# Kernel optimization log

Measured on AMD Instinct MI355X. Metric: run time of the kernel, lower is better.

The kernel has to match this reference:

```python
import jax, jax.numpy as jnp
import numpy as np

D = 512      # embedding_dimension
L1 = 1024    # english sentence length
L2 = 1024    # french sentence length
V1 = 32000   # english vocab
V2 = 32000   # french vocab
NNEG = 8192  # negative samples
SCALE = 0.05 # param init scale (keeps exp() stable)


def setup_inputs() -> dict:
    key = jax.random.key(0)
    ks = jax.random.split(key, 32)
    def n(k, shape):
        return jax.random.normal(k, shape, dtype=jnp.float32) * SCALE
    inp = {}
    inp["en"] = jax.random.randint(ks[0], (L1,), 0, V1)
    inp["fr"] = jax.random.randint(ks[1], (L2,), 0, V2)
    inp["en_neg"] = jax.random.randint(ks[2], (NNEG,), 0, V1)
    inp["fr_neg"] = jax.random.randint(ks[3], (NNEG,), 0, V2)
    # input embeddings
    inp["emb"] = n(ks[4], (V1, D))
    # 3-layer BiLSTM, hidden=D per direction; layer0 in=D, layers 1-2 in=2D
    inp["Wih0"] = n(ks[5], (2, 4 * D, D)); inp["Whh0"] = n(ks[6], (2, 4 * D, D)); inp["b0"] = n(ks[7], (2, 4 * D))
    inp["Wih1"] = n(ks[8], (2, 4 * D, 2 * D)); inp["Whh1"] = n(ks[9], (2, 4 * D, D)); inp["b1"] = n(ks[10], (2, 4 * D))
    inp["Wih2"] = n(ks[11], (2, 4 * D, 2 * D)); inp["Whh2"] = n(ks[12], (2, 4 * D, D)); inp["b2"] = n(ks[13], (2, 4 * D))
    # inference nets (mu and sigma, 2-layer each)
    inp["Wmu1"] = n(ks[14], (D, D)); inp["bmu1"] = n(ks[15], (D,))
    inp["Wmu2"] = n(ks[16], (D, D)); inp["bmu2"] = n(ks[17], (D,))
    inp["Ws1"] = n(ks[18], (D, D)); inp["bs1"] = n(ks[19], (D,))
    inp["Ws2"] = n(ks[20], (D, D)); inp["bs2"] = n(ks[21], (D,))
    # softmax-approximation embedding tables
    inp["E_en"] = n(ks[22], (V1, D))
    inp["E_fr"] = n(ks[23], (V2, D))
    # reparameterization noise (epsilon.sample() per token, made explicit)
    inp["eps"] = jax.random.normal(ks[24], (L1, D), dtype=jnp.float32)
    return inp


def _lstm_bidir(xs, Wih, Whh, b):
    # xs: (L, in); Wih: (2, 4D, in); Whh: (2, 4D, D); b: (2, 4D)
    def run(d, reverse):
        Wi, Wh, bb = Wih[d], Whh[d], b[d]
        def step(carry, x):
            h, c = carry
            g = Wi @ x + Wh @ h + bb
            i, f, gg, o = jnp.split(g, 4)
            i = jax.nn.sigmoid(i); f = jax.nn.sigmoid(f)
            gg = jnp.tanh(gg); o = jax.nn.sigmoid(o)
            c = f * c + i * gg
            h = o * jnp.tanh(c)
            return (h, c), h
        init = (jnp.zeros((Wh.shape[1],), xs.dtype), jnp.zeros((Wh.shape[1],), xs.dtype))
        _, hs = jax.lax.scan(step, init, xs, reverse=reverse)
        return hs
    return run(0, False), run(1, True)  # each (L, D)


def reference(en, fr, en_neg, fr_neg, emb,
              Wih0, Whh0, b0, Wih1, Whh1, b1, Wih2, Whh2, b2,
              Wmu1, bmu1, Wmu2, bmu2, Ws1, bs1, Ws2, bs2,
              E_en, E_fr, eps):
    x = emb[en]                                   # (L1, D)
    hf, hb = _lstm_bidir(x, Wih0, Whh0, b0)
    hf, hb = _lstm_bidir(jnp.concatenate([hf, hb], -1), Wih1, Whh1, b1)
    hf, hb = _lstm_bidir(jnp.concatenate([hf, hb], -1), Wih2, Whh2, b2)
    h = hf + hb                                   # fwd+bwd hidden sum (intermediate[0][0]+intermediate[0][1])
    mu = jax.nn.relu(h @ Wmu1.T + bmu1) @ Wmu2.T + bmu2
    sigma = jax.nn.softplus(jax.nn.relu(h @ Ws1.T + bs1) @ Ws2.T + bs2)
    z = mu + eps * sigma                          # reparameterized sample (L1, D)
    # closed-form KL( N(mu, diag(sigma^2)) || N(0, I) ), summed over tokens
    kl = 0.5 * jnp.sum(sigma ** 2 + mu ** 2 - 1.0 - 2.0 * jnp.log(sigma))
    # english negative-sampling softmax approximation, summed over tokens
    pos = jnp.exp(jnp.sum(z * E_en[en], axis=-1))            # (L1,)
    neg = jnp.sum(jnp.exp(z @ E_en[en_neg].T), axis=-1)      # (L1,)
    sum_x = jnp.sum(pos / (pos + neg))
    # alignment scoring: every french token vs every english latent z
    s = jnp.exp(z @ E_fr[fr].T)                               # (L1, L2)
    negf = jnp.sum(jnp.exp(z @ E_fr[fr_neg].T), -1, keepdims=True)  # (L1, 1)
    p = s / (s + negf)                                        # (L1, L2)
    sum_y = jnp.sum(p) / L1                                   # uniform-alignment marginal
    return -(sum_x + sum_y - kl)


if __name__ == "__main__":
    out = reference(**setup_inputs())
    print(out)
```

## Files before the change

kernel.cpp:

```cpp
#include <hip/hip_runtime.h>
#include <hip/hip_bf16.h>


template<bool GATHER, bool RELU, int EPI>
__global__ __launch_bounds__(256) void gemm_nt(
    const float* __restrict__ A, const float* __restrict__ B,
    const float* __restrict__ bias, const int* __restrict__ idx,
    float* __restrict__ C, const float* __restrict__ negf,
    float* __restrict__ outsum, int M, int N, int K)
{
    __shared__ float As[16][68];
    __shared__ float Bs[16][68];
    __shared__ float wsum[4];

    const int tid = threadIdx.x;
    const int bm = blockIdx.x, bn = blockIdx.y;
    const int tx = tid & 15, ty = tid >> 4;
    const int lr = tid >> 2;
    const int lk = (tid & 3) * 4;

    const long arow = (long)bm * 64 + lr;
    const int  brow = bn * 64 + lr;
    const long bsrc = GATHER ? (long)idx[brow] : (long)brow;
    const float* Ap = A + arow * K + lk;
    const float* Bp = B + bsrc * K + lk;

    float acc[4][4] = {};

    for (int k0 = 0; k0 < K; k0 += 16) {
        float4 av = *(const float4*)(Ap + k0);
        float4 bv = *(const float4*)(Bp + k0);
        __syncthreads();
        As[lk + 0][lr] = av.x; As[lk + 1][lr] = av.y;
        As[lk + 2][lr] = av.z; As[lk + 3][lr] = av.w;
        Bs[lk + 0][lr] = bv.x; Bs[lk + 1][lr] = bv.y;
        Bs[lk + 2][lr] = bv.z; Bs[lk + 3][lr] = bv.w;
        __syncthreads();
#pragma unroll
        for (int k = 0; k < 16; ++k) {
            float4 a = *(const float4*)&As[k][ty * 4];
            float4 b = *(const float4*)&Bs[k][tx * 4];
            float ar[4] = {a.x, a.y, a.z, a.w};
            float br[4] = {b.x, b.y, b.z, b.w};
#pragma unroll
            for (int i = 0; i < 4; ++i)
#pragma unroll
                for (int j = 0; j < 4; ++j)
                    acc[i][j] += ar[i] * br[j];
        }
    }

    const int row0 = bm * 64 + ty * 4, col0 = bn * 64 + tx * 4;

    if (EPI == 0) {
#pragma unroll
        for (int i = 0; i < 4; ++i) {
            float4 v;
            float vv[4];
#pragma unroll
            for (int j = 0; j < 4; ++j) {
                float x = acc[i][j];
                if (bias) x += bias[col0 + j];
                if (RELU) x = x > 0.f ? x : 0.f;
                vv[j] = x;
            }
            v.x = vv[0]; v.y = vv[1]; v.z = vv[2]; v.w = vv[3];
            *(float4*)&C[(long)(row0 + i) * N + col0] = v;
        }
    } else if (EPI == 1) {
#pragma unroll
        for (int i = 0; i < 4; ++i) {
            float s = expf(acc[i][0]) + expf(acc[i][1]) +
                      expf(acc[i][2]) + expf(acc[i][3]);
            s += __shfl_xor(s, 1); s += __shfl_xor(s, 2);
            s += __shfl_xor(s, 4); s += __shfl_xor(s, 8);
            if (tx == 0) atomicAdd(&C[row0 + i], s);
        }
    } else {
        float t = 0.f;
#pragma unroll
        for (int i = 0; i < 4; ++i) {
            float nf = negf[row0 + i];
#pragma unroll
            for (int j = 0; j < 4; ++j) {
                float e = expf(acc[i][j]);
                t += e / (e + nf);
            }
        }
#pragma unroll
        for (int o = 1; o < 64; o <<= 1) t += __shfl_xor(t, o);
        if ((tid & 63) == 0) wsum[tid >> 6] = t;
        __syncthreads();
        if (tid == 0) atomicAdd(outsum, wsum[0] + wsum[1] + wsum[2] + wsum[3]);
    }
}

__global__ __launch_bounds__(256, 1) void lstm_scan(
    const float* __restrict__ Xf, const float* __restrict__ Xb,
    const float* __restrict__ Whh,
    float* __restrict__ out,
    unsigned long long* __restrict__ hbuf)
{
    const int tid  = threadIdx.x;
    const int dir  = blockIdx.x >> 7;
    const int w    = blockIdx.x & 127;
    const int r    = tid >> 4;
    const int ck   = tid & 15;
    const int gate = r >> 2;
    const int jl   = r & 3;
    const int j    = w * 4 + jl;
    const int grow = gate * 512 + j;

    __shared__ float Wl[256 * 36];
    __shared__ float hs[16 * 36];
    __shared__ float ga[16];

    {
        const float4* Wrow = (const float4*)(Whh + ((long)dir * 2048 + grow) * 512 + ck * 32);
        float4* wl4s = (float4*)Wl + tid * 9;
#pragma unroll
        for (int q = 0; q < 8; ++q) wl4s[q] = Wrow[q];
    }
    __syncthreads();

    const float* Xp = dir ? Xb : Xf;
    unsigned long long* myh = hbuf + dir * 4096;

    const int poff = (tid >> 2) * 16 + (tid & 3);

    float c = 0.f;
    bool dead = false;

    const float4* wl4 = (const float4*)Wl + tid * 9;
    const float4* hs4 = (const float4*)hs + ck * 9;

    for (int s = 0; s < 1024; ++s) {
        const int t = dir ? (1023 - s) : s;
        float xg = Xp[(long)t * 2048 + grow];

        unsigned long long* rb = myh + ((s + 1) & 1) * 2048;
        unsigned long long v0, v1;
        unsigned it = 0;
        for (;;) {
            v0 = __hip_atomic_load(&rb[poff],        __ATOMIC_RELAXED, __HIP_MEMORY_SCOPE_AGENT);
            v1 = __hip_atomic_load(&rb[poff + 1024], __ATOMIC_RELAXED, __HIP_MEMORY_SCOPE_AGENT);
            if (dead || ((int)(v0 >> 32) == s && (int)(v1 >> 32) == s)) break;
            if (++it > (1u << 20)) { dead = true; break; }
        }
        hs[((tid) >> 5) * 36 + (tid & 31)]             = __uint_as_float((unsigned)v0);
        hs[((tid + 256) >> 5) * 36 + (tid & 31)]       = __uint_as_float((unsigned)v1);
        __syncthreads();

        float a0 = 0.f, a1 = 0.f;
#pragma unroll
        for (int q = 0; q < 8; q += 2) {
            float4 w0 = wl4[q],     h0 = hs4[q];
            float4 w1 = wl4[q + 1], h1 = hs4[q + 1];
            a0 += w0.x*h0.x + w0.y*h0.y + w0.z*h0.z + w0.w*h0.w;
            a1 += w1.x*h1.x + w1.y*h1.y + w1.z*h1.z + w1.w*h1.w;
        }
        float acc = a0 + a1;
        acc += __shfl_xor(acc, 1);
        acc += __shfl_xor(acc, 2);
        acc += __shfl_xor(acc, 4);
        acc += __shfl_xor(acc, 8);
        if (ck == 0) ga[r] = acc + xg;
        __syncthreads();

        if (tid < 4) {
            float gi = ga[tid], gf = ga[4 + tid], gg = ga[8 + tid], go = ga[12 + tid];
            float i_ = 1.f / (1.f + __expf(-gi));
            float f_ = 1.f / (1.f + __expf(-gf));
            float eg = __expf(2.f * gg);
            float g_ = (eg - 1.f) / (eg + 1.f);
            float o_ = 1.f / (1.f + __expf(-go));
            c = f_ * c + i_ * g_;
            float ec = __expf(2.f * c);
            float tc = (ec - 1.f) / (ec + 1.f);
            float h = o_ * tc;
            unsigned long long pk = (unsigned long long)__float_as_uint(h)
                                  | ((unsigned long long)(unsigned)(s + 1) << 32);
            __hip_atomic_store(&myh[(s & 1) * 2048 + w * 16 + tid], pk,
                               __ATOMIC_RELAXED, __HIP_MEMORY_SCOPE_AGENT);
            out[(long)t * 1024 + dir * 512 + w * 4 + tid] = h;
        }
    }
}

__global__ __launch_bounds__(128) void gather_emb(
    const int* __restrict__ en, const float* __restrict__ emb, float* __restrict__ x0)
{
    const int t = blockIdx.x;
    ((float4*)(x0 + (long)t * 512))[threadIdx.x] =
        ((const float4*)(emb + (long)en[t] * 512))[threadIdx.x];
}

__global__ __launch_bounds__(256) void add_h(
    const float* __restrict__ o2, float* __restrict__ h)
{
    const long i = (long)blockIdx.x * 256 + threadIdx.x;
    const long t = i >> 9, j = i & 511;
    h[i] = o2[t * 1024 + j] + o2[t * 1024 + 512 + j];
}

__global__ __launch_bounds__(256) void zkl_kernel(
    const float* __restrict__ mu, const float* __restrict__ sp,
    const float* __restrict__ eps, float* __restrict__ z, float* __restrict__ klsum)
{
    __shared__ float w4[4];
    const int i = blockIdx.x * 256 + threadIdx.x;
    float m = mu[i], x = sp[i];
    float sg = (x > 20.f) ? x : log1pf(expf(x));
    z[i] = m + eps[i] * sg;
    float kl = 0.5f * (sg * sg + m * m - 1.f) - logf(sg);
#pragma unroll
    for (int o = 1; o < 64; o <<= 1) kl += __shfl_xor(kl, o);
    if ((threadIdx.x & 63) == 0) w4[threadIdx.x >> 6] = kl;
    __syncthreads();
    if (threadIdx.x == 0) atomicAdd(klsum, w4[0] + w4[1] + w4[2] + w4[3]);
}

__global__ __launch_bounds__(64) void pos_kernel(
    const float* __restrict__ z, const float* __restrict__ E_en,
    const int* __restrict__ en, float* __restrict__ pos)
{
    const int t = blockIdx.x, lane = threadIdx.x;
    const float4* zr = (const float4*)(z + (long)t * 512);
    const float4* er = (const float4*)(E_en + (long)en[t] * 512);
    float s = 0.f;
#pragma unroll
    for (int q = 0; q < 2; ++q) {
        float4 a = zr[lane + q * 64], b = er[lane + q * 64];
        s += a.x * b.x + a.y * b.y + a.z * b.z + a.w * b.w;
    }
#pragma unroll
    for (int o = 1; o < 64; o <<= 1) s += __shfl_xor(s, o);
    if (lane == 0) pos[t] = expf(s);
}

__global__ __launch_bounds__(256) void finalize_kernel(
    const float* __restrict__ pos, const float* __restrict__ neg,
    const float* __restrict__ scal, float* __restrict__ out)
{
    __shared__ float w4[4];
    const int tid = threadIdx.x;
    float s = 0.f;
#pragma unroll
    for (int q = 0; q < 4; ++q) {
        int t = tid + q * 256;
        s += pos[t] / (pos[t] + neg[t]);
    }
#pragma unroll
    for (int o = 1; o < 64; o <<= 1) s += __shfl_xor(s, o);
    if ((tid & 63) == 0) w4[tid >> 6] = s;
    __syncthreads();
    if (tid == 0) {
        float sum_x = w4[0] + w4[1] + w4[2] + w4[3];
        out[0] = scal[0] - sum_x - scal[1] * (1.f / 1024.f);
    }
}

extern "C" void kernel_launch(void* const* d_in, const int* in_sizes, int n_in,
                              void* d_out, int out_size, void* d_ws, size_t ws_size,
                              hipStream_t stream)
{
    const int*   en     = (const int*)d_in[0];
    const int*   fr     = (const int*)d_in[1];
    const int*   en_neg = (const int*)d_in[2];
    const int*   fr_neg = (const int*)d_in[3];
    const float* emb    = (const float*)d_in[4];
    const float* Wih0   = (const float*)d_in[5];
    const float* Whh0   = (const float*)d_in[6];
    const float* b0     = (const float*)d_in[7];
    const float* Wih1   = (const float*)d_in[8];
    const float* Whh1   = (const float*)d_in[9];
    const float* b1     = (const float*)d_in[10];
    const float* Wih2   = (const float*)d_in[11];
    const float* Whh2   = (const float*)d_in[12];
    const float* b2     = (const float*)d_in[13];
    const float* Wmu1   = (const float*)d_in[14];
    const float* bmu1   = (const float*)d_in[15];
    const float* Wmu2   = (const float*)d_in[16];
    const float* bmu2   = (const float*)d_in[17];
    const float* Ws1    = (const float*)d_in[18];
    const float* bs1    = (const float*)d_in[19];
    const float* Ws2    = (const float*)d_in[20];
    const float* bs2    = (const float*)d_in[21];
    const float* E_en   = (const float*)d_in[22];
    const float* E_fr   = (const float*)d_in[23];
    const float* eps    = (const float*)d_in[24];
    float* out = (float*)d_out;

    float* w = (float*)d_ws;
    float* x0   = w;  w += 1024 * 512;
    float* bufA = w;  w += 1024 * 1024;
    float* bufB = w;  w += 1024 * 1024;
    float* Xf   = w;  w += 1024 * 2048;
    float* Xb   = w;  w += 1024 * 2048;
    float* h    = w;  w += 1024 * 512;
    float* tmp  = w;  w += 1024 * 512;
    float* mu   = w;  w += 1024 * 512;
    float* sp   = w;  w += 1024 * 512;
    float* z    = w;  w += 1024 * 512;
    float* pos  = w;  w += 1024;
    float* neg  = w;  w += 1024;
    float* negf = w;  w += 1024;
    unsigned long long* hbuf = (unsigned long long*)w; w += 16384;
    float* scal = w;  w += 2;

    hipMemsetAsync(neg, 0, 2048 * sizeof(float), stream);
    hipMemsetAsync(scal, 0, 2 * sizeof(float), stream);

    gather_emb<<<1024, 128, 0, stream>>>(en, emb, x0);

    gemm_nt<false, false, 0><<<dim3(16, 32), 256, 0, stream>>>(
        x0, Wih0,               b0,        nullptr, Xf, nullptr, nullptr, 1024, 2048, 512);
    gemm_nt<false, false, 0><<<dim3(16, 32), 256, 0, stream>>>(
        x0, Wih0 + 2048 * 512,  b0 + 2048, nullptr, Xb, nullptr, nullptr, 1024, 2048, 512);
    hipMemsetAsync(hbuf, 0, 8192 * 8, stream);
    lstm_scan<<<256, 256, 0, stream>>>(Xf, Xb, Whh0, bufA, hbuf);

    gemm_nt<false, false, 0><<<dim3(16, 32), 256, 0, stream>>>(
        bufA, Wih1,               b1,        nullptr, Xf, nullptr, nullptr, 1024, 2048, 1024);
    gemm_nt<false, false, 0><<<dim3(16, 32), 256, 0, stream>>>(
        bufA, Wih1 + 2048 * 1024, b1 + 2048, nullptr, Xb, nullptr, nullptr, 1024, 2048, 1024);
    hipMemsetAsync(hbuf, 0, 8192 * 8, stream);
    lstm_scan<<<256, 256, 0, stream>>>(Xf, Xb, Whh1, bufB, hbuf);

    gemm_nt<false, false, 0><<<dim3(16, 32), 256, 0, stream>>>(
        bufB, Wih2,               b2,        nullptr, Xf, nullptr, nullptr, 1024, 2048, 1024);
    gemm_nt<false, false, 0><<<dim3(16, 32), 256, 0, stream>>>(
        bufB, Wih2 + 2048 * 1024, b2 + 2048, nullptr, Xb, nullptr, nullptr, 1024, 2048, 1024);
    hipMemsetAsync(hbuf, 0, 8192 * 8, stream);
    lstm_scan<<<256, 256, 0, stream>>>(Xf, Xb, Whh2, bufA, hbuf);

    add_h<<<2048, 256, 0, stream>>>(bufA, h);

    gemm_nt<false, true, 0><<<dim3(16, 8), 256, 0, stream>>>(
        h,   Wmu1, bmu1, nullptr, tmp, nullptr, nullptr, 1024, 512, 512);
    gemm_nt<false, false, 0><<<dim3(16, 8), 256, 0, stream>>>(
        tmp, Wmu2, bmu2, nullptr, mu,  nullptr, nullptr, 1024, 512, 512);
    gemm_nt<false, true, 0><<<dim3(16, 8), 256, 0, stream>>>(
        h,   Ws1,  bs1,  nullptr, tmp, nullptr, nullptr, 1024, 512, 512);
    gemm_nt<false, false, 0><<<dim3(16, 8), 256, 0, stream>>>(
        tmp, Ws2,  bs2,  nullptr, sp,  nullptr, nullptr, 1024, 512, 512);

    zkl_kernel<<<2048, 256, 0, stream>>>(mu, sp, eps, z, scal);

    pos_kernel<<<1024, 64, 0, stream>>>(z, E_en, en, pos);
    gemm_nt<true, false, 1><<<dim3(16, 128), 256, 0, stream>>>(
        z, E_en, nullptr, en_neg, neg,  nullptr, nullptr, 1024, 8192, 512);
    gemm_nt<true, false, 1><<<dim3(16, 128), 256, 0, stream>>>(
        z, E_fr, nullptr, fr_neg, negf, nullptr, nullptr, 1024, 8192, 512);
    gemm_nt<true, false, 2><<<dim3(16, 16), 256, 0, stream>>>(
        z, E_fr, nullptr, fr,     nullptr, negf, scal + 1, 1024, 1024, 512);

    finalize_kernel<<<1, 256, 0, stream>>>(pos, neg, scal, out);
}
```

Measured before the change: 7.212 ms.

## Replace tagged double-buffer LSTM handoff with per-step NaN-sentinel history buffer

The recurrent scan exchanged hidden states through a double-buffered array of 64-bit (value, step-tag) words, so each thread polled two words per step. It now writes each step's h into a full per-timestep history buffer pre-filled with an all-ones (NaN) sentinel. Each thread polls a single 64-bit word holding two adjacent floats, halving the polling traffic and the payload size. The cost is extra workspace and large memsets (about 12 MB) per call, and a real h whose bits equal 0xFFFFFFFF would be mistaken for not-yet-written.

```diff
diff --git a/kernel.cpp b/kernel.cpp
--- a/kernel.cpp
+++ b/kernel.cpp
@@ -99,7 +99,7 @@
     const float* __restrict__ Xf, const float* __restrict__ Xb,
     const float* __restrict__ Whh,
     float* __restrict__ out,
-    unsigned long long* __restrict__ hbuf)
+    float* __restrict__ hstep)
 {
     const int tid  = threadIdx.x;
     const int dir  = blockIdx.x >> 7;
@@ -124,9 +124,10 @@
     __syncthreads();
 
     const float* Xp = dir ? Xb : Xf;
-    unsigned long long* myh = hbuf + dir * 4096;
-
-    const int poff = (tid >> 2) * 16 + (tid & 3);
+    float* hrow = hstep + (long)dir * 524800;
+
+    const int i0 = 2 * tid;
+    const int hsi = (i0 >> 5) * 36 + (i0 & 31);
 
     float c = 0.f;
     bool dead = false;
@@ -138,17 +139,19 @@
         const int t = dir ? (1023 - s) : s;
         float xg = Xp[(long)t * 2048 + grow];
 
-        unsigned long long* rb = myh + ((s + 1) & 1) * 2048;
-        unsigned long long v0, v1;
+        const unsigned long long* rp =
+            (const unsigned long long*)(hrow + (long)s * 512) + tid;
+        unsigned long long v;
         unsigned it = 0;
         for (;;) {
-            v0 = __hip_atomic_load(&rb[poff],        __ATOMIC_RELAXED, __HIP_MEMORY_SCOPE_AGENT);
-            v1 = __hip_atomic_load(&rb[poff + 1024], __ATOMIC_RELAXED, __HIP_MEMORY_SCOPE_AGENT);
-            if (dead || ((int)(v0 >> 32) == s && (int)(v1 >> 32) == s)) break;
+            v = __hip_atomic_load(rp, __ATOMIC_RELAXED, __HIP_MEMORY_SCOPE_AGENT);
+            if (((unsigned)v != 0xFFFFFFFFu) &&
+                ((unsigned)(v >> 32) != 0xFFFFFFFFu)) break;
+            if (dead) break;
             if (++it > (1u << 20)) { dead = true; break; }
         }
-        hs[((tid) >> 5) * 36 + (tid & 31)]             = __uint_as_float((unsigned)v0);
-        hs[((tid + 256) >> 5) * 36 + (tid & 31)]       = __uint_as_float((unsigned)v1);
+        hs[hsi]     = __uint_as_float((unsigned)v);
+        hs[hsi + 1] = __uint_as_float((unsigned)(v >> 32));
         __syncthreads();
 
         float a0 = 0.f, a1 = 0.f;
@@ -178,9 +181,7 @@
             float ec = __expf(2.f * c);
             float tc = (ec - 1.f) / (ec + 1.f);
             float h = o_ * tc;
-            unsigned long long pk = (unsigned long long)__float_as_uint(h)
-                                  | ((unsigned long long)(unsigned)(s + 1) << 32);
-            __hip_atomic_store(&myh[(s & 1) * 2048 + w * 16 + tid], pk,
+            __hip_atomic_store(hrow + (long)(s + 1) * 512 + w * 4 + tid, h,
                                __ATOMIC_RELAXED, __HIP_MEMORY_SCOPE_AGENT);
             out[(long)t * 1024 + dir * 512 + w * 4 + tid] = h;
         }
@@ -305,34 +306,40 @@
     float* pos  = w;  w += 1024;
     float* neg  = w;  w += 1024;
     float* negf = w;  w += 1024;
-    unsigned long long* hbuf = (unsigned long long*)w; w += 16384;
+    float* hst0 = w;  w += 2 * 1025 * 512;
+    float* hst1 = w;  w += 2 * 1025 * 512;
+    float* hst2 = w;  w += 2 * 1025 * 512;
     float* scal = w;  w += 2;
 
     hipMemsetAsync(neg, 0, 2048 * sizeof(float), stream);
     hipMemsetAsync(scal, 0, 2 * sizeof(float), stream);
 
+    float* hsts[3] = {hst0, hst1, hst2};
+    for (int k = 0; k < 3; ++k) {
+        hipMemsetAsync(hsts[k], 0xFF, 2 * 1025 * 512 * sizeof(float), stream);
+        hipMemsetAsync(hsts[k],             0, 512 * sizeof(float), stream);
+        hipMemsetAsync(hsts[k] + 1025 * 512, 0, 512 * sizeof(float), stream);
+    }
+
     gather_emb<<<1024, 128, 0, stream>>>(en, emb, x0);
 
     gemm_nt<false, false, 0><<<dim3(16, 32), 256, 0, stream>>>(
         x0, Wih0,               b0,        nullptr, Xf, nullptr, nullptr, 1024, 2048, 512);
     gemm_nt<false, false, 0><<<dim3(16, 32), 256, 0, stream>>>(
         x0, Wih0 + 2048 * 512,  b0 + 2048, nullptr, Xb, nullptr, nullptr, 1024, 2048, 512);
-    hipMemsetAsync(hbuf, 0, 8192 * 8, stream);
-    lstm_scan<<<256, 256, 0, stream>>>(Xf, Xb, Whh0, bufA, hbuf);
+    lstm_scan<<<256, 256, 0, stream>>>(Xf, Xb, Whh0, bufA, hst0);
 
     gemm_nt<false, false, 0><<<dim3(16, 32), 256, 0, stream>>>(
         bufA, Wih1,               b1,        nullptr, Xf, nullptr, nullptr, 1024, 2048, 1024);
     gemm_nt<false, false, 0><<<dim3(16, 32), 256, 0, stream>>>(
         bufA, Wih1 + 2048 * 1024, b1 + 2048, nullptr, Xb, nullptr, nullptr, 1024, 2048, 1024);
-    hipMemsetAsync(hbuf, 0, 8192 * 8, stream);
-    lstm_scan<<<256, 256, 0, stream>>>(Xf, Xb, Whh1, bufB, hbuf);
+    lstm_scan<<<256, 256, 0, stream>>>(Xf, Xb, Whh1, bufB, hst1);
 
     gemm_nt<false, false, 0><<<dim3(16, 32), 256, 0, stream>>>(
         bufB, Wih2,               b2,        nullptr, Xf, nullptr, nullptr, 1024, 2048, 1024);
     gemm_nt<false, false, 0><<<dim3(16, 32), 256, 0, stream>>>(
         bufB, Wih2 + 2048 * 1024, b2 + 2048, nullptr, Xb, nullptr, nullptr, 1024, 2048, 1024);
-    hipMemsetAsync(hbuf, 0, 8192 * 8, stream);
-    lstm_scan<<<256, 256, 0, stream>>>(Xf, Xb, Whh2, bufA, hbuf);
+    lstm_scan<<<256, 256, 0, stream>>>(Xf, Xb, Whh2, bufA, hst2);
 
     add_h<<<2048, 256, 0, stream>>>(bufA, h);
 
```

Result: slower. 8.381 ms (+16.2%).
